# Performance work log

Hardware: AMD Instinct MI355X
Metric: run time of the kernel (lower is better)

## Reference

```python
import jax, jax.numpy as jnp
import numpy as np

N_NODES = 100000
N_EDGES = 1600000
IN_DIM = 128
HID = 96
N_CLASSES = 16
BN_EPS = 1e-5
GIN_EPS = 0.0  # DGL GINConv default init_eps=0, learn_eps=False


def setup_inputs() -> dict:
    key = jax.random.key(0)
    ks = jax.random.split(key, 16)
    d = {}
    d["h"] = jax.random.normal(ks[0], (N_NODES, IN_DIM), dtype=jnp.float32)
    d["src"] = jax.random.randint(ks[1], (N_EDGES,), 0, N_NODES, dtype=jnp.int32)
    d["dst"] = jax.random.randint(ks[2], (N_EDGES,), 0, N_NODES, dtype=jnp.int32)
    # embedding_h: Linear(input_dim, hidden)
    d["W_emb"] = jax.random.normal(ks[3], (IN_DIM, HID), dtype=jnp.float32) / np.sqrt(IN_DIM)
    d["b_emb"] = jnp.zeros((HID,), dtype=jnp.float32)
    # GIN layer 1: MLP(1 layer) Linear(hid,hid) + BN(hid)
    d["W1"] = jax.random.normal(ks[4], (HID, HID), dtype=jnp.float32) / np.sqrt(HID)
    d["b1"] = jnp.zeros((HID,), dtype=jnp.float32)
    d["g1"] = jnp.ones((HID,), dtype=jnp.float32)
    d["be1"] = jnp.zeros((HID,), dtype=jnp.float32)
    # GIN layer 2
    d["W2"] = jax.random.normal(ks[5], (HID, HID), dtype=jnp.float32) / np.sqrt(HID)
    d["b2"] = jnp.zeros((HID,), dtype=jnp.float32)
    d["g2"] = jnp.ones((HID,), dtype=jnp.float32)
    d["be2"] = jnp.zeros((HID,), dtype=jnp.float32)
    # readout: Linear(hid, n_classes)
    d["Wr"] = jax.random.normal(ks[6], (HID, N_CLASSES), dtype=jnp.float32) / np.sqrt(HID)
    d["br"] = jnp.zeros((N_CLASSES,), dtype=jnp.float32)
    return d


def _gin_layer(h, src, dst, W, b, gamma, beta):
    # sum aggregation over incoming edges: agg[v] = sum_{(u,v) in E} h[u]
    agg = jax.ops.segment_sum(h[src], dst, num_segments=N_NODES)
    z = ((1.0 + GIN_EPS) * h + agg) @ W + b           # MLP (single linear)
    mu = jnp.mean(z, axis=0)                            # BatchNorm1d (batch stats)
    var = jnp.var(z, axis=0)
    z = (z - mu) * jax.lax.rsqrt(var + BN_EPS) * gamma + beta
    return jax.nn.relu(z)


def reference(h, src, dst, W_emb, b_emb, W1, b1, g1, be1, W2, b2, g2, be2, Wr, br):
    h = h @ W_emb + b_emb                               # embedding_h
    h = _gin_layer(h, src, dst, W1, b1, g1, be1)        # dropout treated as identity (eval)
    h = _gin_layer(h, src, dst, W2, b2, g2, be2)
    logits = h @ Wr + br                                # readout
    return jax.nn.log_softmax(logits, axis=1)
```

## Files before the change

### kernel.cpp

```cpp
#include <hip/hip_runtime.h>
#include <cmath>

#define N_NODES 100000
#define N_EDGES 1600000
#define IN_DIM 128
#define HID 96
#define NCLS 16
#define NB_GATH 2560

#define BSHIFT 7
#define BNODES 128
#define NBUK 782
#define TILE_E 8192
#define NBLK_E 196
#define NBLK_Q 24
#define NBLK_R 4

typedef unsigned int uint;
typedef unsigned short ushort;
typedef __attribute__((ext_vector_type(8))) short short8v;
typedef __attribute__((ext_vector_type(4))) float float4v;

__device__ __forceinline__ ushort f2bf(float x) {
    uint b = __float_as_uint(x);
    uint r = (b + 0x7FFFu + ((b >> 16) & 1u)) >> 16;
    return (ushort)r;
}
__device__ __forceinline__ float bf2f(ushort u) {
    return __uint_as_float(((uint)u) << 16);
}
__device__ __forceinline__ float bf_lo(uint w) { return __uint_as_float(w << 16); }
__device__ __forceinline__ float bf_hi(uint w) { return __uint_as_float(w & 0xFFFF0000u); }
__device__ __forceinline__ uint pack2bf(float a, float b) {
    return (uint)f2bf(a) | ((uint)f2bf(b) << 16);
}

__device__ __forceinline__ int tile_of(int blk) {
    int xcd = blk & 7, slot = blk >> 3;
    return (xcd < NBLK_R) ? xcd * (NBLK_Q + 1) + slot
                          : NBLK_R * (NBLK_Q + 1) + (xcd - NBLK_R) * NBLK_Q + slot;
}

__global__ __launch_bounds__(256) void wfuse(const float* __restrict__ W_emb,
                                             const float* __restrict__ W1,
                                             const float* __restrict__ b_emb,
                                             float* __restrict__ Wf,
                                             float* __restrict__ bf) {
    __shared__ float W1s[HID * HID];
    for (int i = threadIdx.x; i < HID * HID / 4; i += 256)
        ((float4*)W1s)[i] = ((const float4*)W1)[i];
    __syncthreads();
    int idx = blockIdx.x * 256 + threadIdx.x;
    if (idx < IN_DIM * HID) {
        int i = idx / HID, j = idx - (idx / HID) * HID;
        float acc = 0.f;
        for (int k = 0; k < HID; ++k)
            acc = fmaf(W_emb[(size_t)i * HID + k], W1s[k * HID + j], acc);
        Wf[idx] = acc;
    }
    if (idx < HID) {
        float acc = 0.f;
        for (int k = 0; k < HID; ++k)
            acc = fmaf(b_emb[k], W1s[k * HID + idx], acc);
        bf[idx] = acc;
    }
}

__global__ __launch_bounds__(384) void gemm_l1(const float* __restrict__ X,
                                               const float* __restrict__ W,
                                               const float* __restrict__ bias,
                                               ushort* __restrict__ outB) {
    constexpr int K = IN_DIM, KPAD = K + 8;
    __shared__ ushort A_s[96 * KPAD];
    __shared__ ushort W_t[96 * KPAD];
    __shared__ float bs[HID];
    if (threadIdx.x < HID) bs[threadIdx.x] = bias[threadIdx.x];

    const int rbase = blockIdx.x * 96;
    for (int c = threadIdx.x; c < 96 * (K / 8); c += 384) {
        int row = c / (K / 8), ko = (c - row * (K / 8)) * 8;
        int gr = min(rbase + row, N_NODES - 1);
        const float* xp = X + (size_t)gr * K + ko;
        float4 v0 = *(const float4*)xp;
        float4 v1 = *(const float4*)(xp + 4);
        uint4 p;
        p.x = pack2bf(v0.x, v0.y);
        p.y = pack2bf(v0.z, v0.w);
        p.z = pack2bf(v1.x, v1.y);
        p.w = pack2bf(v1.z, v1.w);
        *(uint4*)&A_s[row * KPAD + ko] = p;
    }
    for (int j = threadIdx.x; j < K * HID; j += 384) {
        int k = j / HID, n = j - k * HID;
        W_t[n * KPAD + k] = f2bf(W[j]);
    }
    __syncthreads();

    const int lane = threadIdx.x & 63, w = threadIdx.x >> 6;
    const int ar = lane & 15, kg = lane >> 4;
    float4v acc[6] = {};
    const ushort* ap = &A_s[(w * 16 + ar) * KPAD + kg * 8];
    const ushort* bp = &W_t[ar * KPAD + kg * 8];
#pragma unroll
    for (int kc = 0; kc < K / 32; ++kc) {
        short8v af = *(const short8v*)(ap + kc * 32);
#pragma unroll
        for (int ct = 0; ct < 6; ++ct) {
            short8v bfv = *(const short8v*)(bp + ct * 16 * KPAD + kc * 32);
            acc[ct] = __builtin_amdgcn_mfma_f32_16x16x32_bf16(af, bfv, acc[ct], 0, 0, 0);
        }
    }
#pragma unroll
    for (int ct = 0; ct < 6; ++ct) {
        int col = ct * 16 + ar;
        float bb = bs[col];
#pragma unroll
        for (int i = 0; i < 4; ++i) {
            int grow = rbase + w * 16 + kg * 4 + i;
            if (grow < N_NODES)
                outB[(size_t)grow * HID + col] = f2bf(acc[ct][i] + bb);
        }
    }
}

__global__ __launch_bounds__(384) void gemm_l2(const ushort* __restrict__ X,
                                               const float* __restrict__ W,
                                               const float* __restrict__ scale,
                                               const float* __restrict__ shift,
                                               ushort* __restrict__ outB) {
    constexpr int K = HID, KPAD = K + 8;
    __shared__ ushort A_s[96 * KPAD];
    __shared__ ushort W_t[96 * KPAD];
    __shared__ float scs[HID], shs[HID];
    if (threadIdx.x < HID) {
        scs[threadIdx.x] = scale[threadIdx.x];
        shs[threadIdx.x] = shift[threadIdx.x];
    }
    __syncthreads();

    const int rbase = blockIdx.x * 96;
    for (int c = threadIdx.x; c < 96 * (K / 8); c += 384) {
        int row = c / (K / 8), ko = (c - row * (K / 8)) * 8;
        int gr = min(rbase + row, N_NODES - 1);
        uint4 u = *(const uint4*)(X + (size_t)gr * K + ko);
        float4 sA = *(const float4*)&scs[ko], sB = *(const float4*)&scs[ko + 4];
        float4 hA = *(const float4*)&shs[ko], hB = *(const float4*)&shs[ko + 4];
        float v0 = fmaxf(fmaf(bf_lo(u.x), sA.x, hA.x), 0.f);
        float v1 = fmaxf(fmaf(bf_hi(u.x), sA.y, hA.y), 0.f);
        float v2 = fmaxf(fmaf(bf_lo(u.y), sA.z, hA.z), 0.f);
        float v3 = fmaxf(fmaf(bf_hi(u.y), sA.w, hA.w), 0.f);
        float v4 = fmaxf(fmaf(bf_lo(u.z), sB.x, hB.x), 0.f);
        float v5 = fmaxf(fmaf(bf_hi(u.z), sB.y, hB.y), 0.f);
        float v6 = fmaxf(fmaf(bf_lo(u.w), sB.z, hB.z), 0.f);
        float v7 = fmaxf(fmaf(bf_hi(u.w), sB.w, hB.w), 0.f);
        uint4 p;
        p.x = pack2bf(v0, v1);
        p.y = pack2bf(v2, v3);
        p.z = pack2bf(v4, v5);
        p.w = pack2bf(v6, v7);
        *(uint4*)&A_s[row * KPAD + ko] = p;
    }
    for (int j = threadIdx.x; j < K * HID; j += 384) {
        int k = j / HID, n = j - k * HID;
        W_t[n * KPAD + k] = f2bf(W[j]);
    }
    __syncthreads();

    const int lane = threadIdx.x & 63, w = threadIdx.x >> 6;
    const int ar = lane & 15, kg = lane >> 4;
    float4v acc[6] = {};
    const ushort* ap = &A_s[(w * 16 + ar) * KPAD + kg * 8];
    const ushort* bp = &W_t[ar * KPAD + kg * 8];
#pragma unroll
    for (int kc = 0; kc < K / 32; ++kc) {
        short8v af = *(const short8v*)(ap + kc * 32);
#pragma unroll
        for (int ct = 0; ct < 6; ++ct) {
            short8v bfv = *(const short8v*)(bp + ct * 16 * KPAD + kc * 32);
            acc[ct] = __builtin_amdgcn_mfma_f32_16x16x32_bf16(af, bfv, acc[ct], 0, 0, 0);
        }
    }
#pragma unroll
    for (int ct = 0; ct < 6; ++ct) {
        int col = ct * 16 + ar;
#pragma unroll
        for (int i = 0; i < 4; ++i) {
            int grow = rbase + w * 16 + kg * 4 + i;
            if (grow < N_NODES)
                outB[(size_t)grow * HID + col] = f2bf(acc[ct][i]);
        }
    }
}

__global__ __launch_bounds__(256) void bin_hist(const int* __restrict__ dst,
                                                int* __restrict__ bcnt) {
    int tile = tile_of(blockIdx.x);
    int beg = tile * TILE_E, end = min(beg + TILE_E, N_EDGES);
    __shared__ int cnt[NBUK];
    for (int b = threadIdx.x; b < NBUK; b += 256) cnt[b] = 0;
    __syncthreads();
    for (int i = beg + threadIdx.x * 4; i < end; i += 256 * 4) {
        int4 d = *(const int4*)(dst + i);
        atomicAdd(&cnt[d.x >> BSHIFT], 1);
        atomicAdd(&cnt[d.y >> BSHIFT], 1);
        atomicAdd(&cnt[d.z >> BSHIFT], 1);
        atomicAdd(&cnt[d.w >> BSHIFT], 1);
    }
    __syncthreads();
    for (int b = threadIdx.x; b < NBUK; b += 256) bcnt[(size_t)b * NBLK_E + tile] = cnt[b];
}

__global__ __launch_bounds__(256) void bin_scanA(const int* __restrict__ bcnt,
                                                 int* __restrict__ boff,
                                                 int* __restrict__ btot) {
    int bin = blockIdx.x, t = threadIdx.x;
    __shared__ int tmp[256];
    int v = (t < NBLK_E) ? bcnt[(size_t)bin * NBLK_E + t] : 0;
    tmp[t] = v;
    __syncthreads();
    for (int off = 1; off < 256; off <<= 1) {
        int a = (t >= off) ? tmp[t - off] : 0;
        __syncthreads();
        tmp[t] += a;
        __syncthreads();
    }
    if (t < NBLK_E) boff[(size_t)bin * NBLK_E + t] = tmp[t] - v;
    if (t == NBLK_E - 1) btot[bin] = tmp[t];
}

__global__ __launch_bounds__(1024) void exscan782(const int* __restrict__ in,
                                                  int* __restrict__ out) {
    int t = threadIdx.x;
    __shared__ int tmp[1024];
    int v = (t < NBUK) ? in[t] : 0;
    tmp[t] = v;
    __syncthreads();
    for (int off = 1; off < 1024; off <<= 1) {
        int a = (t >= off) ? tmp[t - off] : 0;
        __syncthreads();
        tmp[t] += a;
        __syncthreads();
    }
    if (t < NBUK) out[t] = tmp[t] - v;
    if (t == 0) out[NBUK] = N_EDGES;
}

__global__ __launch_bounds__(256) void bin_scatter(const int* __restrict__ src,
                                                   const int* __restrict__ dst,
                                                   const int* __restrict__ bbase,
                                                   const int* __restrict__ boff,
                                                   int* __restrict__ ebuf) {
    int tile = tile_of(blockIdx.x);
    int beg = tile * TILE_E, end = min(beg + TILE_E, N_EDGES);
    __shared__ int curs[NBUK];
    for (int b = threadIdx.x; b < NBUK; b += 256)
        curs[b] = bbase[b] + boff[(size_t)b * NBLK_E + tile];
    __syncthreads();
    for (int i = beg + threadIdx.x * 4; i < end; i += 256 * 4) {
        int4 d = *(const int4*)(dst + i);
        int4 s = *(const int4*)(src + i);
#pragma unroll
        for (int e = 0; e < 4; ++e) {
            int dv = e == 0 ? d.x : e == 1 ? d.y : e == 2 ? d.z : d.w;
            int sv = e == 0 ? s.x : e == 1 ? s.y : e == 2 ? s.z : s.w;
            int p = atomicAdd(&curs[dv >> BSHIFT], 1);
            ebuf[p] = (sv << BSHIFT) | (dv & (BNODES - 1));
        }
    }
}

__global__ __launch_bounds__(256) void bucket_finalize(const int* __restrict__ ebuf,
                                                       const int* __restrict__ bbase,
                                                       int* __restrict__ rp,
                                                       int* __restrict__ cols) {
    int b = blockIdx.x;
    int lo = b << BSHIFT;
    __shared__ int cnt[BNODES];
    __shared__ int cur[BNODES];
    if (threadIdx.x < BNODES) cnt[threadIdx.x] = 0;
    __syncthreads();
    int beg = bbase[b], end = bbase[b + 1];
    for (int i = beg + threadIdx.x; i < end; i += 256)
        atomicAdd(&cnt[ebuf[i] & (BNODES - 1)], 1);
    __syncthreads();
    int t = threadIdx.x;
    int val = (t < BNODES) ? cnt[t] : 0;
    if (t < BNODES) cur[t] = val;
    __syncthreads();
    for (int off = 1; off < BNODES; off <<= 1) {
        int a = (t < BNODES && t >= off) ? cur[t - off] : 0;
        __syncthreads();
        if (t < BNODES) cur[t] += a;
        __syncthreads();
    }
    if (t < BNODES) {
        int excl = beg + cur[t] - val;
        if (lo + t < N_NODES) {
            rp[lo + t] = excl;
            if (lo + t == N_NODES - 1) rp[N_NODES] = N_EDGES;
        }
        cur[t] = excl;
    }
    __syncthreads();
    for (int i = beg + threadIdx.x; i < end; i += 256) {
        int v = ebuf[i];
        int p = atomicAdd(&cur[v & (BNODES - 1)], 1);
        cols[p] = v >> BSHIFT;
    }
}

#define GLANES 24
#define GNODES 8

__global__ __launch_bounds__(192) void gather_stats(const ushort* __restrict__ T,
                                                    const int* __restrict__ rp,
                                                    const int* __restrict__ cols,
                                                    const float* __restrict__ bias,
                                                    ushort* __restrict__ z,
                                                    float* __restrict__ psums,
                                                    float* __restrict__ psq) {
    const int q = threadIdx.x % GLANES;
    const int rs = threadIdx.x / GLANES;
    const float4 bias4 = ((const float4*)bias)[q];
    float4 s = make_float4(0.f, 0.f, 0.f, 0.f);
    float4 sq = make_float4(0.f, 0.f, 0.f, 0.f);

#define ADDROW(u)                                                              \
    {                                                                          \
        ushort4 w = *(const ushort4*)(T + (size_t)(u) * HID + q * 4);          \
        a.x += bf2f(w.x); a.y += bf2f(w.y);                                    \
        a.z += bf2f(w.z); a.w += bf2f(w.w);                                    \
    }

    for (int v = blockIdx.x * GNODES + rs; v < N_NODES; v += NB_GATH * GNODES) {
        float4 a = bias4;
        ADDROW(v);
        int beg = rp[v], end = rp[v + 1];
        int j = beg;
        for (; j + 7 < end; j += 8) {
            int u0 = cols[j], u1 = cols[j + 1], u2 = cols[j + 2], u3 = cols[j + 3];
            int u4 = cols[j + 4], u5 = cols[j + 5], u6 = cols[j + 6], u7 = cols[j + 7];
            ADDROW(u0); ADDROW(u1); ADDROW(u2); ADDROW(u3);
            ADDROW(u4); ADDROW(u5); ADDROW(u6); ADDROW(u7);
        }
        for (; j + 3 < end; j += 4) {
            int u0 = cols[j], u1 = cols[j + 1], u2 = cols[j + 2], u3 = cols[j + 3];
            ADDROW(u0); ADDROW(u1); ADDROW(u2); ADDROW(u3);
        }
        for (; j < end; ++j) ADDROW(cols[j]);

        uint2 o;
        o.x = pack2bf(a.x, a.y);
        o.y = pack2bf(a.z, a.w);
        *(uint2*)(z + (size_t)v * HID + q * 4) = o;
        s.x += a.x; s.y += a.y; s.z += a.z; s.w += a.w;
        sq.x = fmaf(a.x, a.x, sq.x);
        sq.y = fmaf(a.y, a.y, sq.y);
        sq.z = fmaf(a.z, a.z, sq.z);
        sq.w = fmaf(a.w, a.w, sq.w);
    }
#undef ADDROW

    __shared__ float4 ls[GNODES][GLANES], lq[GNODES][GLANES];
    ls[rs][q] = s;
    lq[rs][q] = sq;
    __syncthreads();
    if (threadIdx.x < GLANES) {
        float4 S = ls[0][threadIdx.x], Q = lq[0][threadIdx.x];
#pragma unroll
        for (int i = 1; i < GNODES; ++i) {
            S.x += ls[i][threadIdx.x].x; S.y += ls[i][threadIdx.x].y;
            S.z += ls[i][threadIdx.x].z; S.w += ls[i][threadIdx.x].w;
            Q.x += lq[i][threadIdx.x].x; Q.y += lq[i][threadIdx.x].y;
            Q.z += lq[i][threadIdx.x].z; Q.w += lq[i][threadIdx.x].w;
        }
        ((float4*)(psums + (size_t)blockIdx.x * HID))[threadIdx.x] = S;
        ((float4*)(psq + (size_t)blockIdx.x * HID))[threadIdx.x] = Q;
    }
}

__global__ __launch_bounds__(384) void bn_finalize(const float* __restrict__ psums,
                                                   const float* __restrict__ psq,
                                                   const float* __restrict__ g,
                                                   const float* __restrict__ be,
                                                   float* __restrict__ scale,
                                                   float* __restrict__ shift) {
    int c = threadIdx.x % 96, h = threadIdx.x / 96;
    float S = 0.f, Q = 0.f;
    for (int b = h * (NB_GATH / 4); b < (h + 1) * (NB_GATH / 4); ++b) {
        S += psums[(size_t)b * HID + c];
        Q += psq[(size_t)b * HID + c];
    }
    __shared__ float lS[4][96], lQ[4][96];
    lS[h][c] = S;
    lQ[h][c] = Q;
    __syncthreads();
    if (threadIdx.x < 96) {
        S = lS[0][c] + lS[1][c] + lS[2][c] + lS[3][c];
        Q = lQ[0][c] + lQ[1][c] + lQ[2][c] + lQ[3][c];
        float mu = S * (1.0f / N_NODES);
        float var = Q * (1.0f / N_NODES) - mu * mu;
        float rstd = rsqrtf(var + 1e-5f);
        float sc = g[c] * rstd;
        scale[c] = sc;
        shift[c] = be[c] - mu * sc;
    }
}

__global__ __launch_bounds__(256) void readout_kernel(const ushort* __restrict__ X,
                                                      const float* __restrict__ scale,
                                                      const float* __restrict__ shift,
                                                      const float* __restrict__ Wr,
                                                      const float* __restrict__ br,
                                                      float* __restrict__ out) {
    __shared__ float Ws[HID * NCLS];
    __shared__ float XL[16 * 97];
    __shared__ float scs[HID], shs[HID], bs[NCLS];
    for (int i = threadIdx.x; i < HID * NCLS / 4; i += 256)
        ((float4*)Ws)[i] = ((const float4*)Wr)[i];
    if (threadIdx.x < HID) {
        scs[threadIdx.x] = scale[threadIdx.x];
        shs[threadIdx.x] = shift[threadIdx.x];
    }
    if (threadIdx.x < NCLS) bs[threadIdx.x] = br[threadIdx.x];

    int rr = threadIdx.x >> 4, t = threadIdx.x & 15;
    for (int tile = blockIdx.x; tile < N_NODES / 16; tile += gridDim.x) {
        int rbase = tile * 16;
        __syncthreads();
        if (threadIdx.x < 192) {
            int base = threadIdx.x * 8;
            int row = base / HID, col = base - (base / HID) * HID;
            uint4 w = *(const uint4*)(X + (size_t)rbase * HID + base);
            float v[8] = {bf_lo(w.x), bf_hi(w.x), bf_lo(w.y), bf_hi(w.y),
                          bf_lo(w.z), bf_hi(w.z), bf_lo(w.w), bf_hi(w.w)};
#pragma unroll
            for (int e = 0; e < 8; ++e)
                XL[row * 97 + col + e] = fmaxf(fmaf(v[e], scs[col + e], shs[col + e]), 0.f);
        }
        __syncthreads();
        float acc = bs[t];
        const float* xrow = &XL[rr * 97];
#pragma unroll 4
        for (int k = 0; k < HID; ++k) acc = fmaf(xrow[k], Ws[k * NCLS + t], acc);
        float m = acc;
#pragma unroll
        for (int off = 8; off; off >>= 1) m = fmaxf(m, __shfl_xor(m, off, 16));
        float e = expf(acc - m);
        float sum = e;
#pragma unroll
        for (int off = 8; off; off >>= 1) sum += __shfl_xor(sum, off, 16);
        float lse = m + logf(sum);
        out[(size_t)rbase * NCLS + threadIdx.x] = acc - lse;
    }
}

extern "C" void kernel_launch(void* const* d_in, const int* in_sizes, int n_in,
                              void* d_out, int out_size, void* d_ws, size_t ws_size,
                              hipStream_t stream) {
    const float* h     = (const float*)d_in[0];
    const int*   src   = (const int*)d_in[1];
    const int*   dst   = (const int*)d_in[2];
    const float* W_emb = (const float*)d_in[3];
    const float* b_emb = (const float*)d_in[4];
    const float* W1    = (const float*)d_in[5];
    const float* b1    = (const float*)d_in[6];
    const float* g1    = (const float*)d_in[7];
    const float* be1   = (const float*)d_in[8];
    const float* W2    = (const float*)d_in[9];
    const float* b2    = (const float*)d_in[10];
    const float* g2    = (const float*)d_in[11];
    const float* be2   = (const float*)d_in[12];
    const float* Wr    = (const float*)d_in[13];
    const float* br    = (const float*)d_in[14];

    const size_t nh = (size_t)N_NODES * HID;
    ushort* z    = (ushort*)d_ws;
    ushort* T    = z + nh;
    int* rp      = (int*)(T + nh);
    int* cols    = rp + N_NODES + 1;
    int* ebuf    = cols + N_EDGES;
    int* bcnt    = ebuf + N_EDGES;
    int* boff    = bcnt + NBUK * NBLK_E;
    int* btot    = boff + NBUK * NBLK_E;
    int* bbase   = btot + NBUK;
    float* psums = (float*)(bbase + NBUK + 1);
    float* psq   = psums + (size_t)NB_GATH * HID;
    float* scale = psq + (size_t)NB_GATH * HID;
    float* shift = scale + HID;
    float* Wf    = shift + HID;
    float* bf    = Wf + IN_DIM * HID;

    const int blkT = (N_NODES + 95) / 96;

    bin_hist<<<NBLK_E, 256, 0, stream>>>(dst, bcnt);
    bin_scanA<<<NBUK, 256, 0, stream>>>(bcnt, boff, btot);
    exscan782<<<1, 1024, 0, stream>>>(btot, bbase);
    bin_scatter<<<NBLK_E, 256, 0, stream>>>(src, dst, bbase, boff, ebuf);
    bucket_finalize<<<NBUK, 256, 0, stream>>>(ebuf, bbase, rp, cols);
    wfuse<<<(IN_DIM * HID + 255) / 256, 256, 0, stream>>>(W_emb, W1, b_emb, Wf, bf);

    gemm_l1<<<blkT, 384, 0, stream>>>(h, Wf, bf, T);
    gather_stats<<<NB_GATH, 192, 0, stream>>>(T, rp, cols, b1, z, psums, psq);
    bn_finalize<<<1, 384, 0, stream>>>(psums, psq, g1, be1, scale, shift);

    gemm_l2<<<blkT, 384, 0, stream>>>(z, W2, scale, shift, T);
    gather_stats<<<NB_GATH, 192, 0, stream>>>(T, rp, cols, b2, z, psums, psq);
    bn_finalize<<<1, 384, 0, stream>>>(psums, psq, g2, be2, scale, shift);

    readout_kernel<<<2048, 256, 0, stream>>>(z, scale, shift, Wr, br, (float*)d_out);
}
```

Baseline: 310.9 us.

## Shard node features into eight 12-column slabs for XCD-local gathers

The feature matrices T and z are re-laid out as eight column shards of 12 bf16 values, each padded to 16 and stored contiguously per shard. Gather blocks are assigned one shard by blockIdx&7, so each XCD gathers from a 3.2 MB slab that can stay in its local L2 instead of random 192-byte rows across the full matrix. The GEMMs, readout and BN reduction are adapted to the new layout, and cols is read with nontemporal loads. Padding raises the stored bytes by a third, and each edge's cols entry is now read eight times, once per shard, which adds index traffic.

```diff
diff --git a/kernel.cpp b/kernel.cpp
--- a/kernel.cpp
+++ b/kernel.cpp
@@ -7,6 +7,9 @@
 #define HID 96
 #define NCLS 16
 #define NB_GATH 2560
+#define NSHARD 8
+#define SHW 16
+#define GSH ((size_t)N_NODES * SHW)
 
 #define BSHIFT 7
 #define BNODES 128
@@ -25,9 +28,6 @@
     uint b = __float_as_uint(x);
     uint r = (b + 0x7FFFu + ((b >> 16) & 1u)) >> 16;
     return (ushort)r;
-}
-__device__ __forceinline__ float bf2f(ushort u) {
-    return __uint_as_float(((uint)u) << 16);
 }
 __device__ __forceinline__ float bf_lo(uint w) { return __uint_as_float(w << 16); }
 __device__ __forceinline__ float bf_hi(uint w) { return __uint_as_float(w & 0xFFFF0000u); }
@@ -69,7 +69,7 @@
 __global__ __launch_bounds__(384) void gemm_l1(const float* __restrict__ X,
                                                const float* __restrict__ W,
                                                const float* __restrict__ bias,
-                                               ushort* __restrict__ outB) {
+                                               ushort* __restrict__ Tsh) {
     constexpr int K = IN_DIM, KPAD = K + 8;
     __shared__ ushort A_s[96 * KPAD];
     __shared__ ushort W_t[96 * KPAD];
@@ -113,21 +113,28 @@
 #pragma unroll
     for (int ct = 0; ct < 6; ++ct) {
         int col = ct * 16 + ar;
+        int sh = col / 12, lc = col - sh * 12;
         float bb = bs[col];
+        ushort* base = Tsh + (size_t)sh * GSH + lc;
 #pragma unroll
         for (int i = 0; i < 4; ++i) {
             int grow = rbase + w * 16 + kg * 4 + i;
-            if (grow < N_NODES)
-                outB[(size_t)grow * HID + col] = f2bf(acc[ct][i] + bb);
-        }
-    }
-}
-
-__global__ __launch_bounds__(384) void gemm_l2(const ushort* __restrict__ X,
+            if (grow < N_NODES) base[(size_t)grow * SHW] = f2bf(acc[ct][i] + bb);
+        }
+    }
+    for (int i = threadIdx.x; i < 96 * NSHARD; i += 384) {
+        int row = i / NSHARD, s = i - (i / NSHARD) * NSHARD;
+        int grow = rbase + row;
+        if (grow < N_NODES)
+            *(uint2*)(Tsh + (size_t)s * GSH + (size_t)grow * SHW + 12) = make_uint2(0u, 0u);
+    }
+}
+
+__global__ __launch_bounds__(384) void gemm_l2(const ushort* __restrict__ zsh,
                                                const float* __restrict__ W,
                                                const float* __restrict__ scale,
                                                const float* __restrict__ shift,
-                                               ushort* __restrict__ outB) {
+                                               ushort* __restrict__ Tsh) {
     constexpr int K = HID, KPAD = K + 8;
     __shared__ ushort A_s[96 * KPAD];
     __shared__ ushort W_t[96 * KPAD];
@@ -139,26 +146,17 @@
     __syncthreads();
 
     const int rbase = blockIdx.x * 96;
-    for (int c = threadIdx.x; c < 96 * (K / 8); c += 384) {
-        int row = c / (K / 8), ko = (c - row * (K / 8)) * 8;
+    for (int c = threadIdx.x; c < 96 * 24; c += 384) {
+        int row = c / 24, rem = c - row * 24;
+        int s = rem / 3, q = rem - s * 3;
         int gr = min(rbase + row, N_NODES - 1);
-        uint4 u = *(const uint4*)(X + (size_t)gr * K + ko);
-        float4 sA = *(const float4*)&scs[ko], sB = *(const float4*)&scs[ko + 4];
-        float4 hA = *(const float4*)&shs[ko], hB = *(const float4*)&shs[ko + 4];
-        float v0 = fmaxf(fmaf(bf_lo(u.x), sA.x, hA.x), 0.f);
-        float v1 = fmaxf(fmaf(bf_hi(u.x), sA.y, hA.y), 0.f);
-        float v2 = fmaxf(fmaf(bf_lo(u.y), sA.z, hA.z), 0.f);
-        float v3 = fmaxf(fmaf(bf_hi(u.y), sA.w, hA.w), 0.f);
-        float v4 = fmaxf(fmaf(bf_lo(u.z), sB.x, hB.x), 0.f);
-        float v5 = fmaxf(fmaf(bf_hi(u.z), sB.y, hB.y), 0.f);
-        float v6 = fmaxf(fmaf(bf_lo(u.w), sB.z, hB.z), 0.f);
-        float v7 = fmaxf(fmaf(bf_hi(u.w), sB.w, hB.w), 0.f);
-        uint4 p;
-        p.x = pack2bf(v0, v1);
-        p.y = pack2bf(v2, v3);
-        p.z = pack2bf(v4, v5);
-        p.w = pack2bf(v6, v7);
-        *(uint4*)&A_s[row * KPAD + ko] = p;
+        uint2 u = *(const uint2*)(zsh + (size_t)s * GSH + (size_t)gr * SHW + q * 4);
+        int col = s * 12 + q * 4;
+        float v0 = fmaxf(fmaf(bf_lo(u.x), scs[col + 0], shs[col + 0]), 0.f);
+        float v1 = fmaxf(fmaf(bf_hi(u.x), scs[col + 1], shs[col + 1]), 0.f);
+        float v2 = fmaxf(fmaf(bf_lo(u.y), scs[col + 2], shs[col + 2]), 0.f);
+        float v3 = fmaxf(fmaf(bf_hi(u.y), scs[col + 3], shs[col + 3]), 0.f);
+        *(uint2*)&A_s[row * KPAD + col] = make_uint2(pack2bf(v0, v1), pack2bf(v2, v3));
     }
     for (int j = threadIdx.x; j < K * HID; j += 384) {
         int k = j / HID, n = j - k * HID;
@@ -183,12 +181,19 @@
 #pragma unroll
     for (int ct = 0; ct < 6; ++ct) {
         int col = ct * 16 + ar;
+        int sh = col / 12, lc = col - sh * 12;
+        ushort* base = Tsh + (size_t)sh * GSH + lc;
 #pragma unroll
         for (int i = 0; i < 4; ++i) {
             int grow = rbase + w * 16 + kg * 4 + i;
-            if (grow < N_NODES)
-                outB[(size_t)grow * HID + col] = f2bf(acc[ct][i]);
-        }
+            if (grow < N_NODES) base[(size_t)grow * SHW] = f2bf(acc[ct][i]);
+        }
+    }
+    for (int i = threadIdx.x; i < 96 * NSHARD; i += 384) {
+        int row = i / NSHARD, s = i - (i / NSHARD) * NSHARD;
+        int grow = rbase + row;
+        if (grow < N_NODES)
+            *(uint2*)(Tsh + (size_t)s * GSH + (size_t)grow * SHW + 12) = make_uint2(0u, 0u);
     }
 }
 
@@ -309,50 +314,58 @@
     }
 }
 
-#define GLANES 24
-#define GNODES 8
-
-__global__ __launch_bounds__(192) void gather_stats(const ushort* __restrict__ T,
+__global__ __launch_bounds__(192) void gather_stats(const ushort* __restrict__ Tsh,
                                                     const int* __restrict__ rp,
                                                     const int* __restrict__ cols,
                                                     const float* __restrict__ bias,
-                                                    ushort* __restrict__ z,
+                                                    ushort* __restrict__ zsh,
                                                     float* __restrict__ psums,
                                                     float* __restrict__ psq) {
-    const int q = threadIdx.x % GLANES;
-    const int rs = threadIdx.x / GLANES;
-    const float4 bias4 = ((const float4*)bias)[q];
+    const int shard = blockIdx.x & 7;
+    const int chunk = blockIdx.x >> 3;
+    const int q = threadIdx.x % 3, rs = threadIdx.x / 3;
+    const ushort* Ts = Tsh + (size_t)shard * GSH;
+    ushort* zs = zsh + (size_t)shard * GSH;
+    const float4 bias4 = *(const float4*)(bias + shard * 12 + q * 4);
     float4 s = make_float4(0.f, 0.f, 0.f, 0.f);
     float4 sq = make_float4(0.f, 0.f, 0.f, 0.f);
 
 #define ADDROW(u)                                                              \
     {                                                                          \
-        ushort4 w = *(const ushort4*)(T + (size_t)(u) * HID + q * 4);          \
-        a.x += bf2f(w.x); a.y += bf2f(w.y);                                    \
-        a.z += bf2f(w.z); a.w += bf2f(w.w);                                    \
-    }
-
-    for (int v = blockIdx.x * GNODES + rs; v < N_NODES; v += NB_GATH * GNODES) {
+        uint2 wv = *(const uint2*)(Ts + (size_t)(u) * SHW + q * 4);            \
+        a.x += bf_lo(wv.x); a.y += bf_hi(wv.x);                                \
+        a.z += bf_lo(wv.y); a.w += bf_hi(wv.y);                                \
+    }
+#define NTC(j) __builtin_nontemporal_load(cols + (j))
+
+    for (int v = chunk * 64 + rs; v < N_NODES; v += (NB_GATH / 8) * 64) {
         float4 a = bias4;
         ADDROW(v);
         int beg = rp[v], end = rp[v + 1];
         int j = beg;
         for (; j + 7 < end; j += 8) {
-            int u0 = cols[j], u1 = cols[j + 1], u2 = cols[j + 2], u3 = cols[j + 3];
-            int u4 = cols[j + 4], u5 = cols[j + 5], u6 = cols[j + 6], u7 = cols[j + 7];
+            int u0 = NTC(j), u1 = NTC(j + 1), u2 = NTC(j + 2), u3 = NTC(j + 3);
+            int u4 = NTC(j + 4), u5 = NTC(j + 5), u6 = NTC(j + 6), u7 = NTC(j + 7);
             ADDROW(u0); ADDROW(u1); ADDROW(u2); ADDROW(u3);
             ADDROW(u4); ADDROW(u5); ADDROW(u6); ADDROW(u7);
         }
         for (; j + 3 < end; j += 4) {
-            int u0 = cols[j], u1 = cols[j + 1], u2 = cols[j + 2], u3 = cols[j + 3];
+            int u0 = NTC(j), u1 = NTC(j + 1), u2 = NTC(j + 2), u3 = NTC(j + 3);
             ADDROW(u0); ADDROW(u1); ADDROW(u2); ADDROW(u3);
         }
-        for (; j < end; ++j) ADDROW(cols[j]);
-
-        uint2 o;
-        o.x = pack2bf(a.x, a.y);
-        o.y = pack2bf(a.z, a.w);
-        *(uint2*)(z + (size_t)v * HID + q * 4) = o;
+        for (; j < end; ++j) { int u = NTC(j); ADDROW(u); }
+
+        if (q < 2) {
+            *(uint2*)(zs + (size_t)v * SHW + q * 4) =
+                make_uint2(pack2bf(a.x, a.y), pack2bf(a.z, a.w));
+        } else {
+            uint4 o;
+            o.x = pack2bf(a.x, a.y);
+            o.y = pack2bf(a.z, a.w);
+            o.z = 0u;
+            o.w = 0u;
+            *(uint4*)(zs + (size_t)v * SHW + 8) = o;
+        }
         s.x += a.x; s.y += a.y; s.z += a.z; s.w += a.w;
         sq.x = fmaf(a.x, a.x, sq.x);
         sq.y = fmaf(a.y, a.y, sq.y);
@@ -360,22 +373,23 @@
         sq.w = fmaf(a.w, a.w, sq.w);
     }
 #undef ADDROW
-
-    __shared__ float4 ls[GNODES][GLANES], lq[GNODES][GLANES];
-    ls[rs][q] = s;
-    lq[rs][q] = sq;
-    __syncthreads();
-    if (threadIdx.x < GLANES) {
-        float4 S = ls[0][threadIdx.x], Q = lq[0][threadIdx.x];
-#pragma unroll
-        for (int i = 1; i < GNODES; ++i) {
-            S.x += ls[i][threadIdx.x].x; S.y += ls[i][threadIdx.x].y;
-            S.z += ls[i][threadIdx.x].z; S.w += ls[i][threadIdx.x].w;
-            Q.x += lq[i][threadIdx.x].x; Q.y += lq[i][threadIdx.x].y;
-            Q.z += lq[i][threadIdx.x].z; Q.w += lq[i][threadIdx.x].w;
-        }
-        ((float4*)(psums + (size_t)blockIdx.x * HID))[threadIdx.x] = S;
-        ((float4*)(psq + (size_t)blockIdx.x * HID))[threadIdx.x] = Q;
+#undef NTC
+
+    __shared__ float ls[64][12], lq[64][12];
+    ls[rs][q * 4 + 0] = s.x; ls[rs][q * 4 + 1] = s.y;
+    ls[rs][q * 4 + 2] = s.z; ls[rs][q * 4 + 3] = s.w;
+    lq[rs][q * 4 + 0] = sq.x; lq[rs][q * 4 + 1] = sq.y;
+    lq[rs][q * 4 + 2] = sq.z; lq[rs][q * 4 + 3] = sq.w;
+    __syncthreads();
+    if (threadIdx.x < 12) {
+        float S = 0.f, Q = 0.f;
+#pragma unroll 8
+        for (int i = 0; i < 64; ++i) {
+            S += ls[i][threadIdx.x];
+            Q += lq[i][threadIdx.x];
+        }
+        psums[(size_t)blockIdx.x * 12 + threadIdx.x] = S;
+        psq[(size_t)blockIdx.x * 12 + threadIdx.x] = Q;
     }
 }
 
@@ -386,10 +400,12 @@
                                                    float* __restrict__ scale,
                                                    float* __restrict__ shift) {
     int c = threadIdx.x % 96, h = threadIdx.x / 96;
+    int shard = c / 12, lc = c - shard * 12;
     float S = 0.f, Q = 0.f;
-    for (int b = h * (NB_GATH / 4); b < (h + 1) * (NB_GATH / 4); ++b) {
-        S += psums[(size_t)b * HID + c];
-        Q += psq[(size_t)b * HID + c];
+    for (int i = h * (NB_GATH / 32); i < (h + 1) * (NB_GATH / 32); ++i) {
+        size_t b = (size_t)(i * 8 + shard) * 12 + lc;
+        S += psums[b];
+        Q += psq[b];
     }
     __shared__ float lS[4][96], lQ[4][96];
     lS[h][c] = S;
@@ -407,7 +423,7 @@
     }
 }
 
-__global__ __launch_bounds__(256) void readout_kernel(const ushort* __restrict__ X,
+__global__ __launch_bounds__(256) void readout_kernel(const ushort* __restrict__ zsh,
                                                       const float* __restrict__ scale,
                                                       const float* __restrict__ shift,
                                                       const float* __restrict__ Wr,
@@ -428,15 +444,16 @@
     for (int tile = blockIdx.x; tile < N_NODES / 16; tile += gridDim.x) {
         int rbase = tile * 16;
         __syncthreads();
-        if (threadIdx.x < 192) {
-            int base = threadIdx.x * 8;
-            int row = base / HID, col = base - (base / HID) * HID;
-            uint4 w = *(const uint4*)(X + (size_t)rbase * HID + base);
-            float v[8] = {bf_lo(w.x), bf_hi(w.x), bf_lo(w.y), bf_hi(w.y),
-                          bf_lo(w.z), bf_hi(w.z), bf_lo(w.w), bf_hi(w.w)};
-#pragma unroll
-            for (int e = 0; e < 8; ++e)
-                XL[row * 97 + col + e] = fmaxf(fmaf(v[e], scs[col + e], shs[col + e]), 0.f);
+        for (int c = threadIdx.x; c < 16 * 24; c += 256) {
+            int row = c / 24, rem = c - row * 24;
+            int s = rem / 3, q = rem - s * 3;
+            uint2 u = *(const uint2*)(zsh + (size_t)s * GSH +
+                                      (size_t)(rbase + row) * SHW + q * 4);
+            int col = s * 12 + q * 4;
+            XL[row * 97 + col + 0] = fmaxf(fmaf(bf_lo(u.x), scs[col + 0], shs[col + 0]), 0.f);
+            XL[row * 97 + col + 1] = fmaxf(fmaf(bf_hi(u.x), scs[col + 1], shs[col + 1]), 0.f);
+            XL[row * 97 + col + 2] = fmaxf(fmaf(bf_lo(u.y), scs[col + 2], shs[col + 2]), 0.f);
+            XL[row * 97 + col + 3] = fmaxf(fmaf(bf_hi(u.y), scs[col + 3], shs[col + 3]), 0.f);
         }
         __syncthreads();
         float acc = bs[t];
@@ -474,10 +491,9 @@
     const float* Wr    = (const float*)d_in[13];
     const float* br    = (const float*)d_in[14];
 
-    const size_t nh = (size_t)N_NODES * HID;
-    ushort* z    = (ushort*)d_ws;
-    ushort* T    = z + nh;
-    int* rp      = (int*)(T + nh);
+    ushort* zsh  = (ushort*)d_ws;
+    ushort* Tsh  = zsh + NSHARD * GSH;
+    int* rp      = (int*)(Tsh + NSHARD * GSH);
     int* cols    = rp + N_NODES + 1;
     int* ebuf    = cols + N_EDGES;
     int* bcnt    = ebuf + N_EDGES;
@@ -485,8 +501,8 @@
     int* btot    = boff + NBUK * NBLK_E;
     int* bbase   = btot + NBUK;
     float* psums = (float*)(bbase + NBUK + 1);
-    float* psq   = psums + (size_t)NB_GATH * HID;
-    float* scale = psq + (size_t)NB_GATH * HID;
+    float* psq   = psums + (size_t)NB_GATH * 12;
+    float* scale = psq + (size_t)NB_GATH * 12;
     float* shift = scale + HID;
     float* Wf    = shift + HID;
     float* bf    = Wf + IN_DIM * HID;
@@ -500,13 +516,13 @@
     bucket_finalize<<<NBUK, 256, 0, stream>>>(ebuf, bbase, rp, cols);
     wfuse<<<(IN_DIM * HID + 255) / 256, 256, 0, stream>>>(W_emb, W1, b_emb, Wf, bf);
 
-    gemm_l1<<<blkT, 384, 0, stream>>>(h, Wf, bf, T);
-    gather_stats<<<NB_GATH, 192, 0, stream>>>(T, rp, cols, b1, z, psums, psq);
+    gemm_l1<<<blkT, 384, 0, stream>>>(h, Wf, bf, Tsh);
+    gather_stats<<<NB_GATH, 192, 0, stream>>>(Tsh, rp, cols, b1, zsh, psums, psq);
     bn_finalize<<<1, 384, 0, stream>>>(psums, psq, g1, be1, scale, shift);
 
-    gemm_l2<<<blkT, 384, 0, stream>>>(z, W2, scale, shift, T);
-    gather_stats<<<NB_GATH, 192, 0, stream>>>(T, rp, cols, b2, z, psums, psq);
+    gemm_l2<<<blkT, 384, 0, stream>>>(zsh, W2, scale, shift, Tsh);
+    gather_stats<<<NB_GATH, 192, 0, stream>>>(Tsh, rp, cols, b2, zsh, psums, psq);
     bn_finalize<<<1, 384, 0, stream>>>(psums, psq, g2, be2, scale, shift);
 
-    readout_kernel<<<2048, 256, 0, stream>>>(z, scale, shift, Wr, br, (float*)d_out);
-}
+    readout_kernel<<<2048, 256, 0, stream>>>(zsh, scale, shift, Wr, br, (float*)d_out);
+}
```

Result: slower. 411.4 us (+32.3%).
